# Optimization experiments

Measured on AMD Instinct MI355X. Metric: run time of the kernel, lower is better.

Reference implementation:

```python
import jax, jax.numpy as jnp
import numpy as np

DELTA = 1.0

def _lin(x, W, b):
    return x @ W + b

def _node(x, child_c, child_h, Wioux, bioux, Wiouh, biouh, Wfx, bfx, Wfh, bfh):
    # Child-sum TreeLSTM cell. x: [B, D]; child_c, child_h: [B, nc, M]
    h_sum = child_h.sum(axis=1)  # [B, M]
    iou = _lin(x, Wioux, bioux) + _lin(h_sum, Wiouh, biouh)  # [B, 3M]
    i, o, u = jnp.split(iou, 3, axis=-1)
    i, o, u = jax.nn.sigmoid(i), jax.nn.sigmoid(o), jnp.tanh(u)
    # forget gate per child: fh(child_h) + fx(x) broadcast over children
    f = jax.nn.sigmoid(_lin(child_h, Wfh, bfh) + _lin(x, Wfx, bfx)[:, None, :])  # [B, nc, M]
    c = i * u + (f * child_c).sum(axis=1)
    h = o * jnp.tanh(c)
    return c, h

def _treelstm(xs, Wioux, bioux, Wiouh, biouh, Wfx, bfx, Wfh, bfh):
    # xs: [B, 4, D]. Fixed 4-node tree: root = node 3, leaf children = {0,1,2}.
    # All leaves (same depth) are batched into one fused gate GEMM.
    B, _, D = xs.shape
    M = Wfx.shape[1]
    gates = (Wioux, bioux, Wiouh, biouh, Wfx, bfx, Wfh, bfh)
    x_leaf = xs[:, :3].reshape(B * 3, D)
    z = jnp.zeros((B * 3, 1, M), xs.dtype)  # leaves get zero child state
    c_l, h_l = _node(x_leaf, z, z, *gates)
    c_root, h_root = _node(xs[:, 3], c_l.reshape(B, 3, M), h_l.reshape(B, 3, M), *gates)
    return c_root, h_root

def setup_inputs() -> dict:
    key = jax.random.key(0)
    B, L, Lq, V, D, M, H, O = 512, 64, 128, 50000, 512, 512, 256, 30
    ks = jax.random.split(key, 24)
    ri = lambda k, shape: jax.random.randint(k, shape, 0, V)
    rn = lambda k, shape, s: jax.random.normal(k, shape, jnp.float32) * s
    return {
        'q_v': ri(ks[0], (B, L)), 'q_a0': ri(ks[1], (B, L)), 'n_a0': ri(ks[2], (B, L)),
        'q_a1': ri(ks[3], (B, L)), 'n_a1': ri(ks[4], (B, L)), 'q_a2': ri(ks[5], (B, L)),
        'n_a2': ri(ks[6], (B, L)),
        'query': ri(ks[7], (B, Lq)), 'pos': ri(ks[8], (B, Lq)), 'neg': ri(ks[9], (B, Lq)),
        'emb': rn(ks[10], (V, D), 0.02),
        'Wioux': rn(ks[11], (D, 3 * M), D ** -0.5), 'bioux': jnp.zeros((3 * M,), jnp.float32),
        'Wiouh': rn(ks[12], (M, 3 * M), M ** -0.5), 'biouh': jnp.zeros((3 * M,), jnp.float32),
        'Wfx': rn(ks[13], (D, M), D ** -0.5), 'bfx': jnp.zeros((M,), jnp.float32),
        'Wfh': rn(ks[14], (M, M), M ** -0.5), 'bfh': jnp.zeros((M,), jnp.float32),
        'Wwh': rn(ks[15], (M, H), M ** -0.5), 'bwh': jnp.zeros((H,), jnp.float32),
        'Wwp': rn(ks[16], (H, O), H ** -0.5), 'bwp': jnp.zeros((O,), jnp.float32),
    }

def reference(q_v, q_a0, n_a0, q_a1, n_a1, q_a2, n_a2, query, pos, neg,
              emb, Wioux, bioux, Wiouh, biouh, Wfx, bfx, Wfh, bfh, Wwh, bwh, Wwp, bwp):
    D = emb.shape[1]
    pool = lambda ids: emb[ids].mean(axis=1)  # embedding lookup + mean over tokens -> [B, D]
    qv = pool(q_v)
    def trip(qa, na):  # attribute-level triplet hinge loss, per batch row
        return jax.nn.relu(DELTA - (qv * pool(qa)).sum(-1) + (qv * pool(na)).sum(-1))
    loss = trip(q_a0, n_a0) + trip(q_a1, n_a1) + trip(q_a2, n_a2)
    def seq(ids):  # [B, Lq] -> 4 mean-pooled node vectors [B, 4, D]
        e = emb[ids]
        return e.reshape(e.shape[0], 4, -1, D).mean(axis=2)
    gates = (Wioux, bioux, Wiouh, biouh, Wfx, bfx, Wfh, bfh)
    qc, _ = _treelstm(seq(query), *gates)
    pc, _ = _treelstm(seq(pos), *gates)
    nc, _ = _treelstm(seq(neg), *gates)
    sim = lambda l, r: _lin(jax.nn.sigmoid(_lin(l * r, Wwh, bwh)), Wwp, bwp)  # Similarity module
    a = sim(qc, pc).sum(-1)
    b = sim(qc, nc).sum(-1)
    return loss + jax.nn.relu(DELTA - a + b)
```

## Files before the change

kernel.cpp:

```cpp
#include <hip/hip_runtime.h>
#include <hip/hip_bf16.h>


typedef __attribute__((ext_vector_type(8))) short short8;
typedef __attribute__((ext_vector_type(4))) float floatx4;
typedef __attribute__((ext_vector_type(2))) float floatx2;

__device__ inline ushort f2bf(float f) {
    unsigned u = __float_as_uint(f);
    u += 0x7fffu + ((u >> 16) & 1u);
    return (ushort)(u >> 16);
}
__device__ inline float bf2f(ushort u) { return __uint_as_float((unsigned)u << 16); }
__device__ inline float sigm(float x) { return 1.0f / (1.0f + expf(-x)); }

#if defined(__has_builtin)
#if __has_builtin(__builtin_amdgcn_cvt_pk_f32_fp8) && __has_builtin(__builtin_amdgcn_cvt_pk_fp8_f32)
#define HW_FP8 1
#endif
#endif

#ifndef HW_FP8
__device__ inline unsigned enc1(float x) {
    float a = fabsf(x);
    unsigned s = (__float_as_uint(x) >> 31) << 7;
    unsigned b = __float_as_uint(a);
    unsigned uexp = b >> 23;
    if (uexp < 121) {
        int m = (int)(a * 512.0f + 0.5f);
        if (m >= 8) return s | 0x08u;
        return s | (unsigned)m;
    }
    b += 0x00080000u;
    unsigned e = b >> 23;
    if (e > 135u) return s | 0x7Eu;
    return s | ((e - 120u) << 3) | ((b >> 20) & 7u);
}
__device__ inline float dec1(unsigned v) {
    unsigned s = (v >> 7) & 1u, e = (v >> 3) & 15u, m = v & 7u;
    float r = e ? __uint_as_float(((e + 120u) << 23) | (m << 20))
                : (float)m * 0.001953125f;
    return s ? -r : r;
}
#endif

__device__ inline unsigned pk4(float a, float b, float c, float d) {
#ifdef HW_FP8
    int v = 0;
    v = __builtin_amdgcn_cvt_pk_fp8_f32(a, b, v, false);
    v = __builtin_amdgcn_cvt_pk_fp8_f32(c, d, v, true);
    return (unsigned)v;
#else
    return enc1(a) | (enc1(b) << 8) | (enc1(c) << 16) | (enc1(d) << 24);
#endif
}
__device__ inline void dec4_add(unsigned v, float* acc) {
#ifdef HW_FP8
    floatx2 p0 = __builtin_amdgcn_cvt_pk_f32_fp8(v, false);
    floatx2 p1 = __builtin_amdgcn_cvt_pk_f32_fp8(v, true);
    acc[0] += p0[0]; acc[1] += p0[1]; acc[2] += p1[0]; acc[3] += p1[1];
#else
    acc[0] += dec1(v & 255u); acc[1] += dec1((v >> 8) & 255u);
    acc[2] += dec1((v >> 16) & 255u); acc[3] += dec1(v >> 24);
#endif
}

#define GLD16(gp, sp)                                                        \
    __builtin_amdgcn_global_load_lds(                                        \
        (const __attribute__((address_space(1))) unsigned int*)(const void*)(gp), \
        (__attribute__((address_space(3))) unsigned int*)(void*)(sp), 16, 0, 0)

#define FP8_SCALE 64.0f

__global__ __launch_bounds__(256) void prep_all_kernel(
    const float* __restrict__ emb, unsigned char* __restrict__ emb8,
    const float* __restrict__ Wioux, const float* __restrict__ Wiouh,
    const float* __restrict__ Wfh, const float* __restrict__ Wfx,
    const float* __restrict__ Wwh, const float* __restrict__ Wwp,
    const float* __restrict__ bwp,
    ushort* __restrict__ Wcat_t, ushort* __restrict__ Wfh_t,
    ushort* __restrict__ Wfx_t, ushort* __restrict__ Wwh_t,
    float* __restrict__ wsum) {
    __shared__ float tt[32][33];
    int blk = blockIdx.x, tid = threadIdx.x;
    if (blk < 12500) {
        size_t i = ((size_t)blk * 256 + tid) * 8;
        float4 a = *(const float4*)(emb + i);
        float4 b = *(const float4*)(emb + i + 4);
        uint2 o;
        o.x = pk4(a.x * FP8_SCALE, a.y * FP8_SCALE, a.z * FP8_SCALE, a.w * FP8_SCALE);
        o.y = pk4(b.x * FP8_SCALE, b.y * FP8_SCALE, b.z * FP8_SCALE, b.w * FP8_SCALE);
        *(uint2*)(emb8 + i) = o;
        return;
    }
    int tx = tid & 31, ty = tid >> 5;
    if (blk < 14036) {
        int idx = blk - 12500;
        int k0 = (idx & 31) * 32, n0 = (idx >> 5) * 32;
#pragma unroll
        for (int r = 0; r < 4; ++r) {
            int k = k0 + ty + r * 8;
            const float* s = (k < 512) ? Wioux + (size_t)k * 1536
                                       : Wiouh + (size_t)(k - 512) * 1536;
            tt[ty + r * 8][tx] = s[n0 + tx];
        }
        __syncthreads();
#pragma unroll
        for (int r = 0; r < 4; ++r)
            Wcat_t[(size_t)(n0 + ty + r * 8) * 1024 + k0 + tx] = f2bf(tt[tx][ty + r * 8]);
        return;
    }
    if (blk < 14676) {
        const float* W; ushort* Wt; int idx, ncols;
        if (blk < 14292)      { idx = blk - 14036; W = Wfh; Wt = Wfh_t; ncols = 512; }
        else if (blk < 14548) { idx = blk - 14292; W = Wfx; Wt = Wfx_t; ncols = 512; }
        else                  { idx = blk - 14548; W = Wwh; Wt = Wwh_t; ncols = 256; }
        int nt_count = ncols >> 5;
        int k0 = (idx / nt_count) * 32, n0 = (idx % nt_count) * 32;
#pragma unroll
        for (int r = 0; r < 4; ++r)
            tt[ty + r * 8][tx] = W[(size_t)(k0 + ty + r * 8) * ncols + n0 + tx];
        __syncthreads();
#pragma unroll
        for (int r = 0; r < 4; ++r)
            Wt[(size_t)(n0 + ty + r * 8) * 512 + k0 + tx] = f2bf(tt[tx][ty + r * 8]);
        return;
    }
    {
        float s = 0.f;
        for (int o = 0; o < 30; ++o) s += Wwp[tid * 30 + o];
        wsum[tid] = s;
        if (tid == 0) {
            float t = 0.f;
            for (int o = 0; o < 30; ++o) t += bwp[o];
            wsum[256] = t;
        }
    }
}

__global__ __launch_bounds__(256) void mega_gather_kernel(
    const int* __restrict__ q_v,
    const int* __restrict__ qa0, const int* __restrict__ na0,
    const int* __restrict__ qa1, const int* __restrict__ na1,
    const int* __restrict__ qa2, const int* __restrict__ na2,
    const int* __restrict__ query, const int* __restrict__ pos, const int* __restrict__ neg,
    const unsigned char* __restrict__ emb8,
    float* __restrict__ pools, ushort* __restrict__ Xleaf, ushort* __restrict__ XR) {
    __shared__ float sm[256][9];
    int tid = threadIdx.x;
    int c = tid & 63, g = tid >> 6;
    float acc[8] = {};
    if (blockIdx.x < 3584) {
        int s = blockIdx.x >> 9, b = blockIdx.x & 511;
        const int* aptr[7] = {q_v, qa0, na0, qa1, na1, qa2, na2};
        const int* ids = aptr[s] + b * 64 + g * 16;
        uint2 v[16];
#pragma unroll
        for (int t = 0; t < 16; ++t)
            v[t] = *(const uint2*)(emb8 + (size_t)ids[t] * 512 + c * 8);
#pragma unroll
        for (int t = 0; t < 16; ++t) { dec4_add(v[t].x, acc); dec4_add(v[t].y, acc + 4); }
#pragma unroll
        for (int k = 0; k < 8; ++k) sm[tid][k] = acc[k];
        __syncthreads();
        if (tid < 64) {
#pragma unroll
            for (int gg = 1; gg < 4; ++gg)
#pragma unroll
                for (int k = 0; k < 8; ++k) acc[k] += sm[tid + gg * 64][k];
            const float sc = 1.0f / (64.0f * FP8_SCALE);
            float* dst = pools + ((size_t)s * 512 + b) * 512 + tid * 8;
            *(float4*)dst = make_float4(acc[0] * sc, acc[1] * sc, acc[2] * sc, acc[3] * sc);
            *(float4*)(dst + 4) = make_float4(acc[4] * sc, acc[5] * sc, acc[6] * sc, acc[7] * sc);
        }
    } else {
        int idx = blockIdx.x - 3584;
        int t = idx >> 11, rem = idx & 2047, b = rem >> 2, node = rem & 3;
        const int* sptr[3] = {query, pos, neg};
        const int* ids = sptr[t] + b * 128 + node * 32 + g * 8;
        uint2 v[8];
#pragma unroll
        for (int k = 0; k < 8; ++k)
            v[k] = *(const uint2*)(emb8 + (size_t)ids[k] * 512 + c * 8);
#pragma unroll
        for (int k = 0; k < 8; ++k) { dec4_add(v[k].x, acc); dec4_add(v[k].y, acc + 4); }
#pragma unroll
        for (int k = 0; k < 8; ++k) sm[tid][k] = acc[k];
        __syncthreads();
        if (tid < 64) {
#pragma unroll
            for (int gg = 1; gg < 4; ++gg)
#pragma unroll
                for (int k = 0; k < 8; ++k) acc[k] += sm[tid + gg * 64][k];
            const float sc = 1.0f / (32.0f * FP8_SCALE);
            short8 o;
#pragma unroll
            for (int k = 0; k < 8; ++k) o[k] = (short)f2bf(acc[k] * sc);
            if (node < 3) {
                size_t r = ((size_t)(t * 512 + b)) * 3 + node;
                *(short8*)(Xleaf + r * 512 + tid * 8) = o;
            } else {
                size_t r = (size_t)(t * 512 + b);
                *(short8*)(XR + r * 1024 + tid * 8) = o;
            }
        }
    }
}

__device__ inline void cstore(float* C, size_t idx, float v)  { C[idx] = v; }
__device__ inline void cstore(ushort* C, size_t idx, float v) { C[idx] = f2bf(v); }

template <typename OutT>
__device__ __forceinline__ void gemm_body(const ushort* __restrict__ A, int lda,
                                          const ushort* __restrict__ Bt, int ldb,
                                          OutT* __restrict__ C, int ldc, int K,
                                          int bx, int by, ushort* sA, ushort* sB) {
    int tid = threadIdx.x;
    int m0 = bx * 128, n0 = by * 128;
    int w = tid >> 6, lane = tid & 63;
    int wm = (w >> 1) * 64, wn = (w & 1) * 64;
    int l15 = lane & 15, g = lane >> 4;
    int srow = tid >> 2, scol = (tid & 3) * 8;

    const ushort* Ag0 = A + (size_t)(m0 + srow) * lda + scol;
    const ushort* Ag1 = A + (size_t)(m0 + srow + 64) * lda + scol;
    const ushort* Bg0 = Bt + (size_t)(n0 + srow) * ldb + scol;
    const ushort* Bg1 = Bt + (size_t)(n0 + srow + 64) * ldb + scol;

    floatx4 acc[4][4] = {};

    auto stage = [&](int buf, int kb) {
        ushort* dA = sA + buf * 4096;
        ushort* dB = sB + buf * 4096;
        GLD16(Ag0 + kb, dA + w * 512);
        GLD16(Ag1 + kb, dA + 2048 + w * 512);
        GLD16(Bg0 + kb, dB + w * 512);
        GLD16(Bg1 + kb, dB + 2048 + w * 512);
    };

    stage(0, 0);
    __syncthreads();
    int cur = 0;
    for (int kb = 0; kb < K; kb += 32) {
        if (kb + 32 < K) stage(cur ^ 1, kb + 32);
        const ushort* bA = sA + cur * 4096;
        const ushort* bB = sB + cur * 4096;
        short8 af[4], bf[4];
#pragma unroll
        for (int f = 0; f < 4; ++f) {
            af[f] = *(const short8*)(bA + (wm + f * 16 + l15) * 32 + g * 8);
            bf[f] = *(const short8*)(bB + (wn + f * 16 + l15) * 32 + g * 8);
        }
#pragma unroll
        for (int i = 0; i < 4; ++i)
#pragma unroll
            for (int j = 0; j < 4; ++j)
                acc[i][j] = __builtin_amdgcn_mfma_f32_16x16x32_bf16(af[i], bf[j], acc[i][j], 0, 0, 0);
        __syncthreads();
        cur ^= 1;
    }
#pragma unroll
    for (int i = 0; i < 4; ++i)
#pragma unroll
        for (int j = 0; j < 4; ++j) {
            int row = m0 + wm + i * 16 + g * 4;
            int col = n0 + wn + j * 16 + l15;
#pragma unroll
            for (int r = 0; r < 4; ++r)
                cstore(C, (size_t)(row + r) * ldc + col, acc[i][j][r]);
        }
}

__global__ __launch_bounds__(256) void g1_dots_kernel(
    const ushort* __restrict__ Xleaf, const ushort* __restrict__ Wcat_t,
    ushort* __restrict__ IOU_l,
    const float* __restrict__ pools, float* __restrict__ lossv) {
    __shared__ alignas(16) ushort sA[8192];
    __shared__ alignas(16) ushort sB[8192];
    __shared__ float red[6][4];
    int blk = blockIdx.x, tid = threadIdx.x;
    if (blk < 432) {
        gemm_body(Xleaf, 512, Wcat_t, 1024, IOU_l, 1536, 512, blk % 36, blk / 36, sA, sB);
        return;
    }
    int b = blk - 432;
    const float* pq = pools + (size_t)b * 512;
    float q0 = pq[tid], q1 = pq[tid + 256];
    float d[6];
#pragma unroll
    for (int a = 0; a < 6; ++a) {
        const float* pa = pools + ((size_t)(a + 1) * 512 + b) * 512;
        d[a] = q0 * pa[tid] + q1 * pa[tid + 256];
    }
    int lane = tid & 63, wid = tid >> 6;
#pragma unroll
    for (int a = 0; a < 6; ++a) {
        float v = d[a];
        for (int off = 32; off; off >>= 1) v += __shfl_down(v, off);
        if (lane == 0) red[a][wid] = v;
    }
    __syncthreads();
    if (tid == 0) {
        float l = 0.f;
#pragma unroll
        for (int i = 0; i < 3; ++i) {
            float dq = red[2*i][0] + red[2*i][1] + red[2*i][2] + red[2*i][3];
            float dn = red[2*i+1][0] + red[2*i+1][1] + red[2*i+1][2] + red[2*i+1][3];
            l += fmaxf(0.f, 1.f - dq + dn);
        }
        lossv[b] = l;
    }
}

__global__ __launch_bounds__(256) void gemm3_kernel(
    const ushort* __restrict__ h_l, const ushort* __restrict__ XR,
    const ushort* __restrict__ Wfh_t, const ushort* __restrict__ Wfx_t,
    const ushort* __restrict__ Wcat_t,
    ushort* __restrict__ FH, ushort* __restrict__ FX, ushort* __restrict__ IOU_r) {
    __shared__ alignas(16) ushort sA[8192];
    __shared__ alignas(16) ushort sB[8192];
    int r = blockIdx.x;
    if (r < 144)      gemm_body(XR, 1024, Wcat_t, 1024, IOU_r, 1536, 1024, r % 12, r / 12, sA, sB);
    else if (r < 288) { int q = r - 144; gemm_body(h_l, 512, Wfh_t, 512, FH, 512, 512, q % 36, q / 36, sA, sB); }
    else              { int q = r - 288; gemm_body(XR, 1024, Wfx_t, 512, FX, 512, 512, q % 12, q / 12, sA, sB); }
}

__global__ __launch_bounds__(256) void gemm_sim_kernel(
    const float* __restrict__ c_root, const ushort* __restrict__ Wwh_t,
    float* __restrict__ S) {
    __shared__ alignas(16) ushort sA[8192];
    __shared__ alignas(16) ushort sB[8192];
    int tid = threadIdx.x;
    int bx = blockIdx.x & 7, by = blockIdx.x >> 3;
    int m0 = bx * 128, n0 = by * 128;
    int w = tid >> 6, lane = tid & 63;
    int wm = (w >> 1) * 64, wn = (w & 1) * 64;
    int l15 = lane & 15, g = lane >> 4;
    int srow = tid >> 2, scol = (tid & 3) * 8;

    const ushort* Bg0 = Wwh_t + (size_t)(n0 + srow) * 512 + scol;
    const ushort* Bg1 = Wwh_t + (size_t)(n0 + srow + 64) * 512 + scol;

    floatx4 acc[4][4] = {};

    auto stage = [&](int buf, int kb) {
        ushort* dA = sA + buf * 4096;
        ushort* dB = sB + buf * 4096;
        GLD16(Bg0 + kb, dB + w * 512);
        GLD16(Bg1 + kb, dB + 2048 + w * 512);
#pragma unroll
        for (int half = 0; half < 2; ++half) {
            int gr = m0 + srow + half * 64;
            int b = gr & 511, which = gr >> 9;
            const float* qrow = c_root + (size_t)b * 512 + kb + scol;
            const float* orow = c_root + ((size_t)(which + 1) * 512 + b) * 512 + kb + scol;
            float4 q0 = *(const float4*)qrow, q1 = *(const float4*)(qrow + 4);
            float4 o0 = *(const float4*)orow, o1 = *(const float4*)(orow + 4);
            short8 pv;
            pv[0] = (short)f2bf(q0.x * o0.x); pv[1] = (short)f2bf(q0.y * o0.y);
            pv[2] = (short)f2bf(q0.z * o0.z); pv[3] = (short)f2bf(q0.w * o0.w);
            pv[4] = (short)f2bf(q1.x * o1.x); pv[5] = (short)f2bf(q1.y * o1.y);
            pv[6] = (short)f2bf(q1.z * o1.z); pv[7] = (short)f2bf(q1.w * o1.w);
            *(short8*)(dA + (srow + half * 64) * 32 + scol) = pv;
        }
    };

    stage(0, 0);
    __syncthreads();
    int cur = 0;
    for (int kb = 0; kb < 512; kb += 32) {
        if (kb + 32 < 512) stage(cur ^ 1, kb + 32);
        const ushort* bA = sA + cur * 4096;
        const ushort* bB = sB + cur * 4096;
        short8 af[4], bf[4];
#pragma unroll
        for (int f = 0; f < 4; ++f) {
            af[f] = *(const short8*)(bA + (wm + f * 16 + l15) * 32 + g * 8);
            bf[f] = *(const short8*)(bB + (wn + f * 16 + l15) * 32 + g * 8);
        }
#pragma unroll
        for (int i = 0; i < 4; ++i)
#pragma unroll
            for (int j = 0; j < 4; ++j)
                acc[i][j] = __builtin_amdgcn_mfma_f32_16x16x32_bf16(af[i], bf[j], acc[i][j], 0, 0, 0);
        __syncthreads();
        cur ^= 1;
    }
#pragma unroll
    for (int i = 0; i < 4; ++i)
#pragma unroll
        for (int j = 0; j < 4; ++j) {
            int row = m0 + wm + i * 16 + g * 4;
            int col = n0 + wn + j * 16 + l15;
#pragma unroll
            for (int r = 0; r < 4; ++r)
                S[(size_t)(row + r) * 256 + col] = acc[i][j][r];
        }
}


__global__ __launch_bounds__(256) void leaf_act_kernel(
    const ushort* __restrict__ IOU_l, const float* __restrict__ bioux,
    const float* __restrict__ biouh, ushort* __restrict__ c_l,
    ushort* __restrict__ h_l, ushort* __restrict__ XR) {
    int tb = blockIdx.x, tid = threadIdx.x;
#pragma unroll
    for (int half = 0; half < 2; ++half) {
        int m = tid + half * 256;
        float bi = bioux[m] + biouh[m];
        float bo = bioux[m + 512] + biouh[m + 512];
        float bu = bioux[m + 1024] + biouh[m + 1024];
        float hs = 0.f;
#pragma unroll
        for (int leaf = 0; leaf < 3; ++leaf) {
            size_t r = (size_t)tb * 3 + leaf;
            const ushort* row = IOU_l + r * 1536;
            float iv = sigm(bf2f(row[m]) + bi);
            float ov = sigm(bf2f(row[m + 512]) + bo);
            float uv = tanhf(bf2f(row[m + 1024]) + bu);
            float c = iv * uv;
            c_l[r * 512 + m] = f2bf(c);
            float h = ov * tanhf(c);
            h_l[r * 512 + m] = f2bf(h);
            hs += h;
        }
        XR[(size_t)tb * 1024 + 512 + m] = f2bf(hs);
    }
}

__global__ __launch_bounds__(256) void root_act_kernel(
    const ushort* __restrict__ IOU_r, const ushort* __restrict__ FH,
    const ushort* __restrict__ FX, const ushort* __restrict__ c_l,
    const float* __restrict__ bioux, const float* __restrict__ biouh,
    const float* __restrict__ bfx, const float* __restrict__ bfh,
    float* __restrict__ c_root) {
    int r = blockIdx.x, tid = threadIdx.x;
#pragma unroll
    for (int half = 0; half < 2; ++half) {
        int m = tid + half * 256;
        float iv = sigm(bf2f(IOU_r[(size_t)r * 1536 + m]) + bioux[m] + biouh[m]);
        float uv = tanhf(bf2f(IOU_r[(size_t)r * 1536 + 1024 + m]) + bioux[1024 + m] + biouh[1024 + m]);
        float fx = bf2f(FX[(size_t)r * 512 + m]) + bfx[m];
        float c = iv * uv;
#pragma unroll
        for (int k = 0; k < 3; ++k) {
            size_t idx = ((size_t)r * 3 + k) * 512 + m;
            float f = sigm(bf2f(FH[idx]) + bfh[m] + fx);
            c += f * bf2f(c_l[idx]);
        }
        c_root[(size_t)r * 512 + m] = c;
    }
}

__global__ __launch_bounds__(256) void final_kernel(
    const float* __restrict__ S, const float* __restrict__ bwh,
    const float* __restrict__ wsum, const float* __restrict__ loss,
    float* __restrict__ out) {
    int b = blockIdx.x, tid = threadIdx.x;
    float w = wsum[tid];
    float bw = bwh[tid];
    float va = sigm(S[(size_t)b * 256 + tid] + bw) * w;
    float vb = sigm(S[(size_t)(512 + b) * 256 + tid] + bw) * w;
    int lane = tid & 63, wid = tid >> 6;
    for (int off = 32; off; off >>= 1) {
        va += __shfl_down(va, off);
        vb += __shfl_down(vb, off);
    }
    __shared__ float ra[4], rb[4];
    if (lane == 0) { ra[wid] = va; rb[wid] = vb; }
    __syncthreads();
    if (tid == 0) {
        float a  = ra[0] + ra[1] + ra[2] + ra[3] + wsum[256];
        float bb = rb[0] + rb[1] + rb[2] + rb[3] + wsum[256];
        out[b] = loss[b] + fmaxf(0.f, 1.f - a + bb);
    }
}


extern "C" void kernel_launch(void* const* d_in, const int* in_sizes, int n_in,
                              void* d_out, int out_size, void* d_ws, size_t ws_size,
                              hipStream_t stream) {
    const int* q_v   = (const int*)d_in[0];
    const int* q_a0  = (const int*)d_in[1];
    const int* n_a0  = (const int*)d_in[2];
    const int* q_a1  = (const int*)d_in[3];
    const int* n_a1  = (const int*)d_in[4];
    const int* q_a2  = (const int*)d_in[5];
    const int* n_a2  = (const int*)d_in[6];
    const int* query = (const int*)d_in[7];
    const int* pos   = (const int*)d_in[8];
    const int* neg   = (const int*)d_in[9];
    const float* emb   = (const float*)d_in[10];
    const float* Wioux = (const float*)d_in[11];
    const float* bioux = (const float*)d_in[12];
    const float* Wiouh = (const float*)d_in[13];
    const float* biouh = (const float*)d_in[14];
    const float* Wfx   = (const float*)d_in[15];
    const float* bfx   = (const float*)d_in[16];
    const float* Wfh   = (const float*)d_in[17];
    const float* bfh   = (const float*)d_in[18];
    const float* Wwh   = (const float*)d_in[19];
    const float* bwh   = (const float*)d_in[20];
    const float* Wwp   = (const float*)d_in[21];
    const float* bwp   = (const float*)d_in[22];
    float* out = (float*)d_out;

    char* w = (char*)d_ws;
    size_t off = 0;
    auto alloc = [&](size_t bytes) -> void* {
        void* p = (void*)(w + off);
        off = (off + bytes + 255) & ~(size_t)255;
        return p;
    };
    ushort* Wcat_t = (ushort*)alloc((size_t)1536 * 1024 * 2);
    ushort* Wfh_t  = (ushort*)alloc((size_t)512 * 512 * 2);
    ushort* Wfx_t  = (ushort*)alloc((size_t)512 * 512 * 2);
    ushort* Wwh_t  = (ushort*)alloc((size_t)256 * 512 * 2);
    float*  wsum   = (float*) alloc(257 * 4);
    float*  lossv  = (float*) alloc(512 * 4);
    ushort* Xleaf  = (ushort*)alloc((size_t)4608 * 512 * 2);
    ushort* XR     = (ushort*)alloc((size_t)1536 * 1024 * 2);
    size_t xbase = off;
    unsigned char* emb8 = (unsigned char*)alloc((size_t)50000 * 512);
    float* pools        = (float*)        alloc((size_t)7 * 512 * 512 * 4);
    off = xbase;
    ushort* IOU_l  = (ushort*)alloc((size_t)4608 * 1536 * 2);
    ushort* c_l    = (ushort*)alloc((size_t)4608 * 512 * 2);
    ushort* h_l    = (ushort*)alloc((size_t)4608 * 512 * 2);
    ushort* FH     = (ushort*)alloc((size_t)4608 * 512 * 2);
    ushort* FX     = (ushort*)alloc((size_t)1536 * 512 * 2);
    ushort* IOU_r  = (ushort*)alloc((size_t)1536 * 1536 * 2);
    float*  c_root = (float*) alloc((size_t)1536 * 512 * 4);
    float*  S      = (float*) alloc((size_t)1024 * 256 * 4);

    prep_all_kernel<<<14677, 256, 0, stream>>>(emb, emb8, Wioux, Wiouh, Wfh, Wfx, Wwh,
                                               Wwp, bwp, Wcat_t, Wfh_t, Wfx_t, Wwh_t, wsum);
    mega_gather_kernel<<<9728, 256, 0, stream>>>(q_v, q_a0, n_a0, q_a1, n_a1, q_a2, n_a2,
                                                 query, pos, neg, emb8, pools, Xleaf, XR);
    g1_dots_kernel<<<944, 256, 0, stream>>>(Xleaf, Wcat_t, IOU_l, pools, lossv);
    leaf_act_kernel<<<1536, 256, 0, stream>>>(IOU_l, bioux, biouh, c_l, h_l, XR);
    gemm3_kernel<<<336, 256, 0, stream>>>(h_l, XR, Wfh_t, Wfx_t, Wcat_t, FH, FX, IOU_r);
    root_act_kernel<<<1536, 256, 0, stream>>>(IOU_r, FH, FX, c_l, bioux, biouh, bfx, bfh, c_root);
    gemm_sim_kernel<<<16, 256, 0, stream>>>(c_root, Wwh_t, S);
    final_kernel<<<512, 256, 0, stream>>>(S, bwh, wsum, lossv, out);
}
```

Before: 124.5 us.

## Fuse all stages into one persistent cooperative kernel with grid syncs

Replaces the eight separate kernel launches with a single persistent cooperative kernel. Blocks loop over work units for each phase and are separated by grid-wide syncs. The weight transposes move so they run in the same phase as the embedding gather. The aim is to remove per-launch overhead and the drain and fill gaps between stages, at the cost of grid.sync overhead, lower occupancy from a fixed persistent grid, and shared-memory sizing constrained by the largest phase. If the cooperative launch fails, it falls back to separate per-phase kernels.

```diff
diff --git a/kernel.cpp b/kernel.cpp
--- a/kernel.cpp
+++ b/kernel.cpp
@@ -1,5 +1,8 @@
 #include <hip/hip_runtime.h>
 #include <hip/hip_bf16.h>
+#include <hip/hip_cooperative_groups.h>
+
+namespace cg = cooperative_groups;
 
 
 typedef __attribute__((ext_vector_type(8))) short short8;
@@ -72,138 +75,174 @@
 
 #define FP8_SCALE 64.0f
 
-__global__ __launch_bounds__(256) void prep_all_kernel(
-    const float* __restrict__ emb, unsigned char* __restrict__ emb8,
-    const float* __restrict__ Wioux, const float* __restrict__ Wiouh,
-    const float* __restrict__ Wfh, const float* __restrict__ Wfx,
-    const float* __restrict__ Wwh, const float* __restrict__ Wwp,
-    const float* __restrict__ bwp,
-    ushort* __restrict__ Wcat_t, ushort* __restrict__ Wfh_t,
-    ushort* __restrict__ Wfx_t, ushort* __restrict__ Wwh_t,
-    float* __restrict__ wsum) {
-    __shared__ float tt[32][33];
-    int blk = blockIdx.x, tid = threadIdx.x;
-    if (blk < 12500) {
-        size_t i = ((size_t)blk * 256 + tid) * 8;
-        float4 a = *(const float4*)(emb + i);
-        float4 b = *(const float4*)(emb + i + 4);
-        uint2 o;
-        o.x = pk4(a.x * FP8_SCALE, a.y * FP8_SCALE, a.z * FP8_SCALE, a.w * FP8_SCALE);
-        o.y = pk4(b.x * FP8_SCALE, b.y * FP8_SCALE, b.z * FP8_SCALE, b.w * FP8_SCALE);
-        *(uint2*)(emb8 + i) = o;
-        return;
-    }
+#define N_CONV   12500
+#define N_GATHER 9728
+#define N_WPREP  2177
+#define N_PH2    (N_GATHER + N_WPREP)
+#define N_PH3    944
+#define N_LEAF   1536
+#define N_GEMM3  336
+#define N_ROOT   1536
+#define N_SIM    16
+#define N_FINAL  512
+
+struct Params {
+    const int *q_v, *qa0, *na0, *qa1, *na1, *qa2, *na2, *query, *pos, *neg;
+    const float *emb, *Wioux, *bioux, *Wiouh, *biouh, *Wfx, *bfx, *Wfh, *bfh,
+                *Wwh, *bwh, *Wwp, *bwp;
+    float* out;
+    ushort *Wcat_t, *Wfh_t, *Wfx_t, *Wwh_t;
+    float *wsum, *lossv;
+    ushort *Xleaf, *XR;
+    unsigned char* emb8;
+    float* pools;
+    ushort *IOU_l, *c_l, *h_l, *FH, *FX, *IOU_r;
+    float *c_root, *S;
+    int nblk;
+};
+
+
+__device__ __forceinline__ void conv_unit(int blk, int tid, const Params& p) {
+    size_t i = ((size_t)blk * 256 + tid) * 8;
+    float4 a = *(const float4*)(p.emb + i);
+    float4 b = *(const float4*)(p.emb + i + 4);
+    uint2 o;
+    o.x = pk4(a.x * FP8_SCALE, a.y * FP8_SCALE, a.z * FP8_SCALE, a.w * FP8_SCALE);
+    o.y = pk4(b.x * FP8_SCALE, b.y * FP8_SCALE, b.z * FP8_SCALE, b.w * FP8_SCALE);
+    *(uint2*)(p.emb8 + i) = o;
+}
+
+__device__ __forceinline__ void wprep_unit(int blk, int tid, const Params& p, float* tt ) {
     int tx = tid & 31, ty = tid >> 5;
-    if (blk < 14036) {
-        int idx = blk - 12500;
-        int k0 = (idx & 31) * 32, n0 = (idx >> 5) * 32;
+    if (blk < 1536) {
+        int k0 = (blk & 31) * 32, n0 = (blk >> 5) * 32;
 #pragma unroll
         for (int r = 0; r < 4; ++r) {
             int k = k0 + ty + r * 8;
-            const float* s = (k < 512) ? Wioux + (size_t)k * 1536
-                                       : Wiouh + (size_t)(k - 512) * 1536;
-            tt[ty + r * 8][tx] = s[n0 + tx];
+            const float* s = (k < 512) ? p.Wioux + (size_t)k * 1536
+                                       : p.Wiouh + (size_t)(k - 512) * 1536;
+            tt[(ty + r * 8) * 33 + tx] = s[n0 + tx];
         }
         __syncthreads();
 #pragma unroll
         for (int r = 0; r < 4; ++r)
-            Wcat_t[(size_t)(n0 + ty + r * 8) * 1024 + k0 + tx] = f2bf(tt[tx][ty + r * 8]);
+            p.Wcat_t[(size_t)(n0 + ty + r * 8) * 1024 + k0 + tx] = f2bf(tt[tx * 33 + ty + r * 8]);
         return;
     }
-    if (blk < 14676) {
+    if (blk < 2176) {
         const float* W; ushort* Wt; int idx, ncols;
-        if (blk < 14292)      { idx = blk - 14036; W = Wfh; Wt = Wfh_t; ncols = 512; }
-        else if (blk < 14548) { idx = blk - 14292; W = Wfx; Wt = Wfx_t; ncols = 512; }
-        else                  { idx = blk - 14548; W = Wwh; Wt = Wwh_t; ncols = 256; }
+        if (blk < 1792)      { idx = blk - 1536; W = p.Wfh; Wt = p.Wfh_t; ncols = 512; }
+        else if (blk < 2048) { idx = blk - 1792; W = p.Wfx; Wt = p.Wfx_t; ncols = 512; }
+        else                 { idx = blk - 2048; W = p.Wwh; Wt = p.Wwh_t; ncols = 256; }
         int nt_count = ncols >> 5;
         int k0 = (idx / nt_count) * 32, n0 = (idx % nt_count) * 32;
 #pragma unroll
         for (int r = 0; r < 4; ++r)
-            tt[ty + r * 8][tx] = W[(size_t)(k0 + ty + r * 8) * ncols + n0 + tx];
+            tt[(ty + r * 8) * 33 + tx] = W[(size_t)(k0 + ty + r * 8) * ncols + n0 + tx];
         __syncthreads();
 #pragma unroll
         for (int r = 0; r < 4; ++r)
-            Wt[(size_t)(n0 + ty + r * 8) * 512 + k0 + tx] = f2bf(tt[tx][ty + r * 8]);
+            Wt[(size_t)(n0 + ty + r * 8) * 512 + k0 + tx] = f2bf(tt[tx * 33 + ty + r * 8]);
         return;
     }
     {
         float s = 0.f;
-        for (int o = 0; o < 30; ++o) s += Wwp[tid * 30 + o];
-        wsum[tid] = s;
+        for (int o = 0; o < 30; ++o) s += p.Wwp[tid * 30 + o];
+        p.wsum[tid] = s;
         if (tid == 0) {
             float t = 0.f;
-            for (int o = 0; o < 30; ++o) t += bwp[o];
-            wsum[256] = t;
-        }
-    }
-}
-
-__global__ __launch_bounds__(256) void mega_gather_kernel(
-    const int* __restrict__ q_v,
-    const int* __restrict__ qa0, const int* __restrict__ na0,
-    const int* __restrict__ qa1, const int* __restrict__ na1,
-    const int* __restrict__ qa2, const int* __restrict__ na2,
-    const int* __restrict__ query, const int* __restrict__ pos, const int* __restrict__ neg,
-    const unsigned char* __restrict__ emb8,
-    float* __restrict__ pools, ushort* __restrict__ Xleaf, ushort* __restrict__ XR) {
-    __shared__ float sm[256][9];
-    int tid = threadIdx.x;
+            for (int o = 0; o < 30; ++o) t += p.bwp[o];
+            p.wsum[256] = t;
+        }
+    }
+}
+
+__device__ __forceinline__ void gather_unit(int blk, int tid, const Params& p, float* sm) {
     int c = tid & 63, g = tid >> 6;
     float acc[8] = {};
-    if (blockIdx.x < 3584) {
-        int s = blockIdx.x >> 9, b = blockIdx.x & 511;
-        const int* aptr[7] = {q_v, qa0, na0, qa1, na1, qa2, na2};
+    if (blk < 3584) {
+        int s = blk >> 9, b = blk & 511;
+        const int* aptr[7] = {p.q_v, p.qa0, p.na0, p.qa1, p.na1, p.qa2, p.na2};
         const int* ids = aptr[s] + b * 64 + g * 16;
         uint2 v[16];
 #pragma unroll
         for (int t = 0; t < 16; ++t)
-            v[t] = *(const uint2*)(emb8 + (size_t)ids[t] * 512 + c * 8);
+            v[t] = *(const uint2*)(p.emb8 + (size_t)ids[t] * 512 + c * 8);
 #pragma unroll
         for (int t = 0; t < 16; ++t) { dec4_add(v[t].x, acc); dec4_add(v[t].y, acc + 4); }
 #pragma unroll
-        for (int k = 0; k < 8; ++k) sm[tid][k] = acc[k];
+        for (int k = 0; k < 8; ++k) sm[tid * 9 + k] = acc[k];
         __syncthreads();
         if (tid < 64) {
 #pragma unroll
             for (int gg = 1; gg < 4; ++gg)
 #pragma unroll
-                for (int k = 0; k < 8; ++k) acc[k] += sm[tid + gg * 64][k];
+                for (int k = 0; k < 8; ++k) acc[k] += sm[(tid + gg * 64) * 9 + k];
             const float sc = 1.0f / (64.0f * FP8_SCALE);
-            float* dst = pools + ((size_t)s * 512 + b) * 512 + tid * 8;
+            float* dst = p.pools + ((size_t)s * 512 + b) * 512 + tid * 8;
             *(float4*)dst = make_float4(acc[0] * sc, acc[1] * sc, acc[2] * sc, acc[3] * sc);
             *(float4*)(dst + 4) = make_float4(acc[4] * sc, acc[5] * sc, acc[6] * sc, acc[7] * sc);
         }
     } else {
-        int idx = blockIdx.x - 3584;
+        int idx = blk - 3584;
         int t = idx >> 11, rem = idx & 2047, b = rem >> 2, node = rem & 3;
-        const int* sptr[3] = {query, pos, neg};
+        const int* sptr[3] = {p.query, p.pos, p.neg};
         const int* ids = sptr[t] + b * 128 + node * 32 + g * 8;
         uint2 v[8];
 #pragma unroll
         for (int k = 0; k < 8; ++k)
-            v[k] = *(const uint2*)(emb8 + (size_t)ids[k] * 512 + c * 8);
+            v[k] = *(const uint2*)(p.emb8 + (size_t)ids[k] * 512 + c * 8);
 #pragma unroll
         for (int k = 0; k < 8; ++k) { dec4_add(v[k].x, acc); dec4_add(v[k].y, acc + 4); }
 #pragma unroll
-        for (int k = 0; k < 8; ++k) sm[tid][k] = acc[k];
+        for (int k = 0; k < 8; ++k) sm[tid * 9 + k] = acc[k];
         __syncthreads();
         if (tid < 64) {
 #pragma unroll
             for (int gg = 1; gg < 4; ++gg)
 #pragma unroll
-                for (int k = 0; k < 8; ++k) acc[k] += sm[tid + gg * 64][k];
+                for (int k = 0; k < 8; ++k) acc[k] += sm[(tid + gg * 64) * 9 + k];
             const float sc = 1.0f / (32.0f * FP8_SCALE);
             short8 o;
 #pragma unroll
             for (int k = 0; k < 8; ++k) o[k] = (short)f2bf(acc[k] * sc);
             if (node < 3) {
                 size_t r = ((size_t)(t * 512 + b)) * 3 + node;
-                *(short8*)(Xleaf + r * 512 + tid * 8) = o;
+                *(short8*)(p.Xleaf + r * 512 + tid * 8) = o;
             } else {
                 size_t r = (size_t)(t * 512 + b);
-                *(short8*)(XR + r * 1024 + tid * 8) = o;
+                *(short8*)(p.XR + r * 1024 + tid * 8) = o;
             }
         }
+    }
+}
+
+__device__ __forceinline__ void dots_unit(int b, int tid, const Params& p, float* red ) {
+    const float* pq = p.pools + (size_t)b * 512;
+    float q0 = pq[tid], q1 = pq[tid + 256];
+    float d[6];
+#pragma unroll
+    for (int a = 0; a < 6; ++a) {
+        const float* pa = p.pools + ((size_t)(a + 1) * 512 + b) * 512;
+        d[a] = q0 * pa[tid] + q1 * pa[tid + 256];
+    }
+    int lane = tid & 63, wid = tid >> 6;
+#pragma unroll
+    for (int a = 0; a < 6; ++a) {
+        float v = d[a];
+        for (int off = 32; off; off >>= 1) v += __shfl_down(v, off);
+        if (lane == 0) red[a * 4 + wid] = v;
+    }
+    __syncthreads();
+    if (tid == 0) {
+        float l = 0.f;
+#pragma unroll
+        for (int i = 0; i < 3; ++i) {
+            float dq = red[2*i*4] + red[2*i*4+1] + red[2*i*4+2] + red[2*i*4+3];
+            float dn = red[(2*i+1)*4] + red[(2*i+1)*4+1] + red[(2*i+1)*4+2] + red[(2*i+1)*4+3];
+            l += fmaxf(0.f, 1.f - dq + dn);
+        }
+        p.lossv[b] = l;
     }
 }
 
@@ -211,9 +250,9 @@
 __device__ inline void cstore(ushort* C, size_t idx, float v) { C[idx] = f2bf(v); }
 
 template <typename OutT>
-__device__ __forceinline__ void gemm_body(const ushort* __restrict__ A, int lda,
-                                          const ushort* __restrict__ Bt, int ldb,
-                                          OutT* __restrict__ C, int ldc, int K,
+__device__ __forceinline__ void gemm_body(const ushort* A, int lda,
+                                          const ushort* Bt, int ldb,
+                                          OutT* C, int ldc, int K,
                                           int bx, int by, ushort* sA, ushort* sB) {
     int tid = threadIdx.x;
     int m0 = bx * 128, n0 = by * 128;
@@ -271,75 +310,83 @@
         }
 }
 
-__global__ __launch_bounds__(256) void g1_dots_kernel(
-    const ushort* __restrict__ Xleaf, const ushort* __restrict__ Wcat_t,
-    ushort* __restrict__ IOU_l,
-    const float* __restrict__ pools, float* __restrict__ lossv) {
-    __shared__ alignas(16) ushort sA[8192];
-    __shared__ alignas(16) ushort sB[8192];
-    __shared__ float red[6][4];
-    int blk = blockIdx.x, tid = threadIdx.x;
-    if (blk < 432) {
-        gemm_body(Xleaf, 512, Wcat_t, 1024, IOU_l, 1536, 512, blk % 36, blk / 36, sA, sB);
-        return;
-    }
-    int b = blk - 432;
-    const float* pq = pools + (size_t)b * 512;
-    float q0 = pq[tid], q1 = pq[tid + 256];
-    float d[6];
-#pragma unroll
-    for (int a = 0; a < 6; ++a) {
-        const float* pa = pools + ((size_t)(a + 1) * 512 + b) * 512;
-        d[a] = q0 * pa[tid] + q1 * pa[tid + 256];
-    }
-    int lane = tid & 63, wid = tid >> 6;
-#pragma unroll
-    for (int a = 0; a < 6; ++a) {
-        float v = d[a];
-        for (int off = 32; off; off >>= 1) v += __shfl_down(v, off);
-        if (lane == 0) red[a][wid] = v;
-    }
-    __syncthreads();
-    if (tid == 0) {
-        float l = 0.f;
-#pragma unroll
-        for (int i = 0; i < 3; ++i) {
-            float dq = red[2*i][0] + red[2*i][1] + red[2*i][2] + red[2*i][3];
-            float dn = red[2*i+1][0] + red[2*i+1][1] + red[2*i+1][2] + red[2*i+1][3];
-            l += fmaxf(0.f, 1.f - dq + dn);
-        }
-        lossv[b] = l;
-    }
-}
-
-__global__ __launch_bounds__(256) void gemm3_kernel(
-    const ushort* __restrict__ h_l, const ushort* __restrict__ XR,
-    const ushort* __restrict__ Wfh_t, const ushort* __restrict__ Wfx_t,
-    const ushort* __restrict__ Wcat_t,
-    ushort* __restrict__ FH, ushort* __restrict__ FX, ushort* __restrict__ IOU_r) {
-    __shared__ alignas(16) ushort sA[8192];
-    __shared__ alignas(16) ushort sB[8192];
-    int r = blockIdx.x;
-    if (r < 144)      gemm_body(XR, 1024, Wcat_t, 1024, IOU_r, 1536, 1024, r % 12, r / 12, sA, sB);
-    else if (r < 288) { int q = r - 144; gemm_body(h_l, 512, Wfh_t, 512, FH, 512, 512, q % 36, q / 36, sA, sB); }
-    else              { int q = r - 288; gemm_body(XR, 1024, Wfx_t, 512, FX, 512, 512, q % 12, q / 12, sA, sB); }
-}
-
-__global__ __launch_bounds__(256) void gemm_sim_kernel(
-    const float* __restrict__ c_root, const ushort* __restrict__ Wwh_t,
-    float* __restrict__ S) {
-    __shared__ alignas(16) ushort sA[8192];
-    __shared__ alignas(16) ushort sB[8192];
-    int tid = threadIdx.x;
-    int bx = blockIdx.x & 7, by = blockIdx.x >> 3;
+__device__ __forceinline__ void phase3_unit(int u, int tid, const Params& p, char* smem) {
+    if (u < 432)
+        gemm_body(p.Xleaf, 512, p.Wcat_t, 1024, p.IOU_l, 1536, 512, u % 36, u / 36,
+                  (ushort*)smem, (ushort*)(smem + 16384));
+    else
+        dots_unit(u - 432, tid, p, (float*)smem);
+}
+
+__device__ __forceinline__ void phase5_unit(int u, const Params& p, char* smem) {
+    ushort* sA = (ushort*)smem;
+    ushort* sB = (ushort*)(smem + 16384);
+    if (u < 144)
+        gemm_body(p.XR, 1024, p.Wcat_t, 1024, p.IOU_r, 1536, 1024, u % 12, u / 12, sA, sB);
+    else if (u < 288) {
+        int q = u - 144;
+        gemm_body(p.h_l, 512, p.Wfh_t, 512, p.FH, 512, 512, q % 36, q / 36, sA, sB);
+    } else {
+        int q = u - 288;
+        gemm_body(p.XR, 1024, p.Wfx_t, 512, p.FX, 512, 512, q % 12, q / 12, sA, sB);
+    }
+}
+
+__device__ __forceinline__ void leaf_unit(int tb, int tid, const Params& p) {
+#pragma unroll
+    for (int half = 0; half < 2; ++half) {
+        int m = tid + half * 256;
+        float bi = p.bioux[m] + p.biouh[m];
+        float bo = p.bioux[m + 512] + p.biouh[m + 512];
+        float bu = p.bioux[m + 1024] + p.biouh[m + 1024];
+        float hs = 0.f;
+#pragma unroll
+        for (int leaf = 0; leaf < 3; ++leaf) {
+            size_t r = (size_t)tb * 3 + leaf;
+            const ushort* row = p.IOU_l + r * 1536;
+            float iv = sigm(bf2f(row[m]) + bi);
+            float ov = sigm(bf2f(row[m + 512]) + bo);
+            float uv = tanhf(bf2f(row[m + 1024]) + bu);
+            float c = iv * uv;
+            p.c_l[r * 512 + m] = f2bf(c);
+            float h = ov * tanhf(c);
+            p.h_l[r * 512 + m] = f2bf(h);
+            hs += h;
+        }
+        p.XR[(size_t)tb * 1024 + 512 + m] = f2bf(hs);
+    }
+}
+
+__device__ __forceinline__ void root_unit(int r, int tid, const Params& p) {
+#pragma unroll
+    for (int half = 0; half < 2; ++half) {
+        int m = tid + half * 256;
+        float iv = sigm(bf2f(p.IOU_r[(size_t)r * 1536 + m]) + p.bioux[m] + p.biouh[m]);
+        float uv = tanhf(bf2f(p.IOU_r[(size_t)r * 1536 + 1024 + m]) + p.bioux[1024 + m] + p.biouh[1024 + m]);
+        float fx = bf2f(p.FX[(size_t)r * 512 + m]) + p.bfx[m];
+        float c = iv * uv;
+#pragma unroll
+        for (int k = 0; k < 3; ++k) {
+            size_t idx = ((size_t)r * 3 + k) * 512 + m;
+            float f = sigm(bf2f(p.FH[idx]) + p.bfh[m] + fx);
+            c += f * bf2f(p.c_l[idx]);
+        }
+        p.c_root[(size_t)r * 512 + m] = c;
+    }
+}
+
+__device__ __forceinline__ void sim_unit(int blk, int tid, const Params& p, char* smem) {
+    ushort* sA = (ushort*)smem;
+    ushort* sB = (ushort*)(smem + 16384);
+    int bx = blk & 7, by = blk >> 3;
     int m0 = bx * 128, n0 = by * 128;
     int w = tid >> 6, lane = tid & 63;
     int wm = (w >> 1) * 64, wn = (w & 1) * 64;
     int l15 = lane & 15, g = lane >> 4;
     int srow = tid >> 2, scol = (tid & 3) * 8;
 
-    const ushort* Bg0 = Wwh_t + (size_t)(n0 + srow) * 512 + scol;
-    const ushort* Bg1 = Wwh_t + (size_t)(n0 + srow + 64) * 512 + scol;
+    const ushort* Bg0 = p.Wwh_t + (size_t)(n0 + srow) * 512 + scol;
+    const ushort* Bg1 = p.Wwh_t + (size_t)(n0 + srow + 64) * 512 + scol;
 
     floatx4 acc[4][4] = {};
 
@@ -352,8 +399,8 @@
         for (int half = 0; half < 2; ++half) {
             int gr = m0 + srow + half * 64;
             int b = gr & 511, which = gr >> 9;
-            const float* qrow = c_root + (size_t)b * 512 + kb + scol;
-            const float* orow = c_root + ((size_t)(which + 1) * 512 + b) * 512 + kb + scol;
+            const float* qrow = p.c_root + (size_t)b * 512 + kb + scol;
+            const float* orow = p.c_root + ((size_t)(which + 1) * 512 + b) * 512 + kb + scol;
             float4 q0 = *(const float4*)qrow, q1 = *(const float4*)(qrow + 4);
             float4 o0 = *(const float4*)orow, o1 = *(const float4*)(orow + 4);
             short8 pv;
@@ -394,153 +441,186 @@
             int col = n0 + wn + j * 16 + l15;
 #pragma unroll
             for (int r = 0; r < 4; ++r)
-                S[(size_t)(row + r) * 256 + col] = acc[i][j][r];
-        }
-}
-
-
-__global__ __launch_bounds__(256) void leaf_act_kernel(
-    const ushort* __restrict__ IOU_l, const float* __restrict__ bioux,
-    const float* __restrict__ biouh, ushort* __restrict__ c_l,
-    ushort* __restrict__ h_l, ushort* __restrict__ XR) {
-    int tb = blockIdx.x, tid = threadIdx.x;
-#pragma unroll
-    for (int half = 0; half < 2; ++half) {
-        int m = tid + half * 256;
-        float bi = bioux[m] + biouh[m];
-        float bo = bioux[m + 512] + biouh[m + 512];
-        float bu = bioux[m + 1024] + biouh[m + 1024];
-        float hs = 0.f;
-#pragma unroll
-        for (int leaf = 0; leaf < 3; ++leaf) {
-            size_t r = (size_t)tb * 3 + leaf;
-            const ushort* row = IOU_l + r * 1536;
-            float iv = sigm(bf2f(row[m]) + bi);
-            float ov = sigm(bf2f(row[m + 512]) + bo);
-            float uv = tanhf(bf2f(row[m + 1024]) + bu);
-            float c = iv * uv;
-            c_l[r * 512 + m] = f2bf(c);
-            float h = ov * tanhf(c);
-            h_l[r * 512 + m] = f2bf(h);
-            hs += h;
-        }
-        XR[(size_t)tb * 1024 + 512 + m] = f2bf(hs);
-    }
-}
-
-__global__ __launch_bounds__(256) void root_act_kernel(
-    const ushort* __restrict__ IOU_r, const ushort* __restrict__ FH,
-    const ushort* __restrict__ FX, const ushort* __restrict__ c_l,
-    const float* __restrict__ bioux, const float* __restrict__ biouh,
-    const float* __restrict__ bfx, const float* __restrict__ bfh,
-    float* __restrict__ c_root) {
-    int r = blockIdx.x, tid = threadIdx.x;
-#pragma unroll
-    for (int half = 0; half < 2; ++half) {
-        int m = tid + half * 256;
-        float iv = sigm(bf2f(IOU_r[(size_t)r * 1536 + m]) + bioux[m] + biouh[m]);
-        float uv = tanhf(bf2f(IOU_r[(size_t)r * 1536 + 1024 + m]) + bioux[1024 + m] + biouh[1024 + m]);
-        float fx = bf2f(FX[(size_t)r * 512 + m]) + bfx[m];
-        float c = iv * uv;
-#pragma unroll
-        for (int k = 0; k < 3; ++k) {
-            size_t idx = ((size_t)r * 3 + k) * 512 + m;
-            float f = sigm(bf2f(FH[idx]) + bfh[m] + fx);
-            c += f * bf2f(c_l[idx]);
-        }
-        c_root[(size_t)r * 512 + m] = c;
-    }
-}
-
-__global__ __launch_bounds__(256) void final_kernel(
-    const float* __restrict__ S, const float* __restrict__ bwh,
-    const float* __restrict__ wsum, const float* __restrict__ loss,
-    float* __restrict__ out) {
-    int b = blockIdx.x, tid = threadIdx.x;
-    float w = wsum[tid];
-    float bw = bwh[tid];
-    float va = sigm(S[(size_t)b * 256 + tid] + bw) * w;
-    float vb = sigm(S[(size_t)(512 + b) * 256 + tid] + bw) * w;
+                p.S[(size_t)(row + r) * 256 + col] = acc[i][j][r];
+        }
+}
+
+__device__ __forceinline__ void final_unit(int b, int tid, const Params& p, float* red ) {
+    float w = p.wsum[tid];
+    float bw = p.bwh[tid];
+    float va = sigm(p.S[(size_t)b * 256 + tid] + bw) * w;
+    float vb = sigm(p.S[(size_t)(512 + b) * 256 + tid] + bw) * w;
     int lane = tid & 63, wid = tid >> 6;
     for (int off = 32; off; off >>= 1) {
         va += __shfl_down(va, off);
         vb += __shfl_down(vb, off);
     }
-    __shared__ float ra[4], rb[4];
-    if (lane == 0) { ra[wid] = va; rb[wid] = vb; }
+    if (lane == 0) { red[wid] = va; red[4 + wid] = vb; }
     __syncthreads();
     if (tid == 0) {
-        float a  = ra[0] + ra[1] + ra[2] + ra[3] + wsum[256];
-        float bb = rb[0] + rb[1] + rb[2] + rb[3] + wsum[256];
-        out[b] = loss[b] + fmaxf(0.f, 1.f - a + bb);
-    }
+        float a  = red[0] + red[1] + red[2] + red[3] + p.wsum[256];
+        float bb = red[4] + red[5] + red[6] + red[7] + p.wsum[256];
+        p.out[b] = p.lossv[b] + fmaxf(0.f, 1.f - a + bb);
+    }
+}
+
+
+__global__ __launch_bounds__(256, 2) void mega_kernel(Params p) {
+    cg::grid_group grid = cg::this_grid();
+    __shared__ __align__(16) char smem[32768];
+    float* smf = (float*)smem;
+    int tid = threadIdx.x;
+    int nblk = p.nblk;
+
+    for (int u = blockIdx.x; u < N_CONV; u += nblk) conv_unit(u, tid, p);
+    grid.sync();
+    for (int u = blockIdx.x; u < N_PH2; u += nblk) {
+        if (u < N_GATHER) gather_unit(u, tid, p, smf);
+        else              wprep_unit(u - N_GATHER, tid, p, smf);
+        __syncthreads();
+    }
+    grid.sync();
+    for (int u = blockIdx.x; u < N_PH3; u += nblk) {
+        phase3_unit(u, tid, p, smem);
+        __syncthreads();
+    }
+    grid.sync();
+    for (int u = blockIdx.x; u < N_LEAF; u += nblk) leaf_unit(u, tid, p);
+    grid.sync();
+    for (int u = blockIdx.x; u < N_GEMM3; u += nblk) {
+        phase5_unit(u, p, smem);
+        __syncthreads();
+    }
+    grid.sync();
+    for (int u = blockIdx.x; u < N_ROOT; u += nblk) root_unit(u, tid, p);
+    grid.sync();
+    for (int u = blockIdx.x; u < N_SIM; u += nblk) {
+        sim_unit(u, tid, p, smem);
+        __syncthreads();
+    }
+    grid.sync();
+    for (int u = blockIdx.x; u < N_FINAL; u += nblk) {
+        final_unit(u, tid, p, smf);
+        __syncthreads();
+    }
+}
+
+
+__global__ __launch_bounds__(256) void conv_kernel(Params p) {
+    conv_unit(blockIdx.x, threadIdx.x, p);
+}
+__global__ __launch_bounds__(256) void gatherprep_kernel(Params p) {
+    __shared__ float sm[256 * 9];
+    int u = blockIdx.x;
+    if (u < N_GATHER) gather_unit(u, threadIdx.x, p, sm);
+    else              wprep_unit(u - N_GATHER, threadIdx.x, p, sm);
+}
+__global__ __launch_bounds__(256) void g1dots_kernel(Params p) {
+    __shared__ __align__(16) char smem[32768];
+    phase3_unit(blockIdx.x, threadIdx.x, p, smem);
+}
+__global__ __launch_bounds__(256) void leaf_kernel(Params p) {
+    leaf_unit(blockIdx.x, threadIdx.x, p);
+}
+__global__ __launch_bounds__(256) void gemm3_kernel(Params p) {
+    __shared__ __align__(16) char smem[32768];
+    phase5_unit(blockIdx.x, p, smem);
+}
+__global__ __launch_bounds__(256) void root_kernel(Params p) {
+    root_unit(blockIdx.x, threadIdx.x, p);
+}
+__global__ __launch_bounds__(256) void sim_kernel(Params p) {
+    __shared__ __align__(16) char smem[32768];
+    sim_unit(blockIdx.x, threadIdx.x, p, smem);
+}
+__global__ __launch_bounds__(256) void final_kernel_w(Params p) {
+    __shared__ float red[8];
+    final_unit(blockIdx.x, threadIdx.x, p, red);
 }
 
 
 extern "C" void kernel_launch(void* const* d_in, const int* in_sizes, int n_in,
                               void* d_out, int out_size, void* d_ws, size_t ws_size,
                               hipStream_t stream) {
-    const int* q_v   = (const int*)d_in[0];
-    const int* q_a0  = (const int*)d_in[1];
-    const int* n_a0  = (const int*)d_in[2];
-    const int* q_a1  = (const int*)d_in[3];
-    const int* n_a1  = (const int*)d_in[4];
-    const int* q_a2  = (const int*)d_in[5];
-    const int* n_a2  = (const int*)d_in[6];
-    const int* query = (const int*)d_in[7];
-    const int* pos   = (const int*)d_in[8];
-    const int* neg   = (const int*)d_in[9];
-    const float* emb   = (const float*)d_in[10];
-    const float* Wioux = (const float*)d_in[11];
-    const float* bioux = (const float*)d_in[12];
-    const float* Wiouh = (const float*)d_in[13];
-    const float* biouh = (const float*)d_in[14];
-    const float* Wfx   = (const float*)d_in[15];
-    const float* bfx   = (const float*)d_in[16];
-    const float* Wfh   = (const float*)d_in[17];
-    const float* bfh   = (const float*)d_in[18];
-    const float* Wwh   = (const float*)d_in[19];
-    const float* bwh   = (const float*)d_in[20];
-    const float* Wwp   = (const float*)d_in[21];
-    const float* bwp   = (const float*)d_in[22];
-    float* out = (float*)d_out;
+    Params prm;
+    prm.q_v   = (const int*)d_in[0];
+    prm.qa0   = (const int*)d_in[1];
+    prm.na0   = (const int*)d_in[2];
+    prm.qa1   = (const int*)d_in[3];
+    prm.na1   = (const int*)d_in[4];
+    prm.qa2   = (const int*)d_in[5];
+    prm.na2   = (const int*)d_in[6];
+    prm.query = (const int*)d_in[7];
+    prm.pos   = (const int*)d_in[8];
+    prm.neg   = (const int*)d_in[9];
+    prm.emb   = (const float*)d_in[10];
+    prm.Wioux = (const float*)d_in[11];
+    prm.bioux = (const float*)d_in[12];
+    prm.Wiouh = (const float*)d_in[13];
+    prm.biouh = (const float*)d_in[14];
+    prm.Wfx   = (const float*)d_in[15];
+    prm.bfx   = (const float*)d_in[16];
+    prm.Wfh   = (const float*)d_in[17];
+    prm.bfh   = (const float*)d_in[18];
+    prm.Wwh   = (const float*)d_in[19];
+    prm.bwh   = (const float*)d_in[20];
+    prm.Wwp   = (const float*)d_in[21];
+    prm.bwp   = (const float*)d_in[22];
+    prm.out   = (float*)d_out;
 
     char* w = (char*)d_ws;
     size_t off = 0;
     auto alloc = [&](size_t bytes) -> void* {
-        void* p = (void*)(w + off);
+        void* ptr = (void*)(w + off);
         off = (off + bytes + 255) & ~(size_t)255;
-        return p;
+        return ptr;
     };
-    ushort* Wcat_t = (ushort*)alloc((size_t)1536 * 1024 * 2);
-    ushort* Wfh_t  = (ushort*)alloc((size_t)512 * 512 * 2);
-    ushort* Wfx_t  = (ushort*)alloc((size_t)512 * 512 * 2);
-    ushort* Wwh_t  = (ushort*)alloc((size_t)256 * 512 * 2);
-    float*  wsum   = (float*) alloc(257 * 4);
-    float*  lossv  = (float*) alloc(512 * 4);
-    ushort* Xleaf  = (ushort*)alloc((size_t)4608 * 512 * 2);
-    ushort* XR     = (ushort*)alloc((size_t)1536 * 1024 * 2);
+    prm.Wcat_t = (ushort*)alloc((size_t)1536 * 1024 * 2);
+    prm.Wfh_t  = (ushort*)alloc((size_t)512 * 512 * 2);
+    prm.Wfx_t  = (ushort*)alloc((size_t)512 * 512 * 2);
+    prm.Wwh_t  = (ushort*)alloc((size_t)256 * 512 * 2);
+    prm.wsum   = (float*) alloc(257 * 4);
+    prm.lossv  = (float*) alloc(512 * 4);
+    prm.Xleaf  = (ushort*)alloc((size_t)4608 * 512 * 2);
+    prm.XR     = (ushort*)alloc((size_t)1536 * 1024 * 2);
     size_t xbase = off;
-    unsigned char* emb8 = (unsigned char*)alloc((size_t)50000 * 512);
-    float* pools        = (float*)        alloc((size_t)7 * 512 * 512 * 4);
+    prm.emb8  = (unsigned char*)alloc((size_t)50000 * 512);
+    prm.pools = (float*)        alloc((size_t)7 * 512 * 512 * 4);
     off = xbase;
-    ushort* IOU_l  = (ushort*)alloc((size_t)4608 * 1536 * 2);
-    ushort* c_l    = (ushort*)alloc((size_t)4608 * 512 * 2);
-    ushort* h_l    = (ushort*)alloc((size_t)4608 * 512 * 2);
-    ushort* FH     = (ushort*)alloc((size_t)4608 * 512 * 2);
-    ushort* FX     = (ushort*)alloc((size_t)1536 * 512 * 2);
-    ushort* IOU_r  = (ushort*)alloc((size_t)1536 * 1536 * 2);
-    float*  c_root = (float*) alloc((size_t)1536 * 512 * 4);
-    float*  S      = (float*) alloc((size_t)1024 * 256 * 4);
-
-    prep_all_kernel<<<14677, 256, 0, stream>>>(emb, emb8, Wioux, Wiouh, Wfh, Wfx, Wwh,
-                                               Wwp, bwp, Wcat_t, Wfh_t, Wfx_t, Wwh_t, wsum);
-    mega_gather_kernel<<<9728, 256, 0, stream>>>(q_v, q_a0, n_a0, q_a1, n_a1, q_a2, n_a2,
-                                                 query, pos, neg, emb8, pools, Xleaf, XR);
-    g1_dots_kernel<<<944, 256, 0, stream>>>(Xleaf, Wcat_t, IOU_l, pools, lossv);
-    leaf_act_kernel<<<1536, 256, 0, stream>>>(IOU_l, bioux, biouh, c_l, h_l, XR);
-    gemm3_kernel<<<336, 256, 0, stream>>>(h_l, XR, Wfh_t, Wfx_t, Wcat_t, FH, FX, IOU_r);
-    root_act_kernel<<<1536, 256, 0, stream>>>(IOU_r, FH, FX, c_l, bioux, biouh, bfx, bfh, c_root);
-    gemm_sim_kernel<<<16, 256, 0, stream>>>(c_root, Wwh_t, S);
-    final_kernel<<<512, 256, 0, stream>>>(S, bwh, wsum, lossv, out);
-}
+    prm.IOU_l  = (ushort*)alloc((size_t)4608 * 1536 * 2);
+    prm.c_l    = (ushort*)alloc((size_t)4608 * 512 * 2);
+    prm.h_l    = (ushort*)alloc((size_t)4608 * 512 * 2);
+    prm.FH     = (ushort*)alloc((size_t)4608 * 512 * 2);
+    prm.FX     = (ushort*)alloc((size_t)1536 * 512 * 2);
+    prm.IOU_r  = (ushort*)alloc((size_t)1536 * 1536 * 2);
+    prm.c_root = (float*) alloc((size_t)1536 * 512 * 4);
+    prm.S      = (float*) alloc((size_t)1024 * 256 * 4);
+
+    int dev = 0;
+    (void)hipGetDevice(&dev);
+    int maxPerCU = 0, nCU = 0;
+    (void)hipOccupancyMaxActiveBlocksPerMultiprocessor(&maxPerCU, (const void*)mega_kernel, 256, 0);
+    (void)hipDeviceGetAttribute(&nCU, hipDeviceAttributeMultiprocessorCount, dev);
+
+    hipError_t err = hipErrorUnknown;
+    if (maxPerCU > 0 && nCU > 0) {
+        int nblk = maxPerCU * nCU;
+        if (nblk > 2048) nblk = 2048;
+        prm.nblk = nblk;
+        void* args[] = {&prm};
+        err = hipLaunchCooperativeKernel((const void*)mega_kernel, dim3(nblk), dim3(256),
+                                         args, 0, stream);
+    }
+    if (err != hipSuccess) {
+        (void)hipGetLastError();
+        prm.nblk = 0;
+        conv_kernel<<<N_CONV, 256, 0, stream>>>(prm);
+        gatherprep_kernel<<<N_PH2, 256, 0, stream>>>(prm);
+        g1dots_kernel<<<N_PH3, 256, 0, stream>>>(prm);
+        leaf_kernel<<<N_LEAF, 256, 0, stream>>>(prm);
+        gemm3_kernel<<<N_GEMM3, 256, 0, stream>>>(prm);
+        root_kernel<<<N_ROOT, 256, 0, stream>>>(prm);
+        sim_kernel<<<N_SIM, 256, 0, stream>>>(prm);
+        final_kernel_w<<<N_FINAL, 256, 0, stream>>>(prm);
+    }
+}
```

Result: slower. 401.5 us (+222.5%).
